# Optimization experiments

Hardware: AMD Instinct MI355X
Metric: run time of the kernel (lower is better)

Reference implementation:

```python
import jax, jax.numpy as jnp
import numpy as np
from jax import lax

D = 256; NH = 8; LYR = 2; G = 64; K = G * G; T = 4; EC = 32
B = 4; N = 512; CITY = 256; DFF = 4 * D

def _conv(x, w):
    return lax.conv_general_dilated(x, w, (1, 1), 'SAME', dimension_numbers=('NCHW', 'OIHW', 'NCHW'))

def _ln(x, w, b):
    m = x.mean(-1, keepdims=True)
    v = ((x - m) ** 2).mean(-1, keepdims=True)
    return (x - m) / jnp.sqrt(v + 1e-5) * w + b

def _mlp(x, w1, b1, w2, b2):
    return jax.nn.gelu(x @ w1 + b1) @ w2 + b2

def setup_inputs():
    key = jax.random.key(0)
    ks = iter(jax.random.split(key, 64))
    def nrm(shape, s=0.02):
        return jax.random.normal(next(ks), shape, jnp.float32) * s
    return {
        'meas_xy': jax.random.uniform(next(ks), (B, N, 2), jnp.float32),
        'meas_v': jax.random.normal(next(ks), (B, N), jnp.float32),
        'bs_xy': jax.random.uniform(next(ks), (B, 1, 2), jnp.float32),
        'task_id': jax.random.randint(next(ks), (B,), 0, T),
        'city': jax.random.uniform(next(ks), (B, CITY, CITY), jnp.float32),
        'mp_w1': nrm((3, D)), 'mp_b1': jnp.zeros((D,)), 'mp_w2': nrm((D, D)), 'mp_b2': jnp.zeros((D,)),
        'bp_w1': nrm((2, D)), 'bp_b1': jnp.zeros((D,)), 'bp_w2': nrm((D, D)), 'bp_b2': jnp.zeros((D,)),
        'env_w1': nrm((EC, 1, 3, 3)), 'env_b1': jnp.zeros((EC,)),
        'env_w2': nrm((EC, EC, 3, 3)), 'env_b2': jnp.zeros((EC,)),
        'env_w3': nrm((D, EC, 1, 1)), 'env_b3': jnp.zeros((D,)),
        'task_emb': nrm((T, D)), 'tp_w': nrm((D, D)), 'tp_b': jnp.zeros((D,)),
        'grid_pos': nrm((K, D)),
        'blk_dens_w': nrm((LYR, D)), 'blk_dens_b': jnp.zeros((LYR, D)),
        'blk_ln1_w': jnp.ones((LYR, D)), 'blk_ln1_b': jnp.zeros((LYR, D)),
        'blk_wq': nrm((LYR, D, D)), 'blk_bq': jnp.zeros((LYR, D)),
        'blk_wk': nrm((LYR, D, D)), 'blk_bk': jnp.zeros((LYR, D)),
        'blk_wv': nrm((LYR, D, D)), 'blk_bv': jnp.zeros((LYR, D)),
        'blk_wo': nrm((LYR, D, D)), 'blk_bo': jnp.zeros((LYR, D)),
        'blk_ln2_w': jnp.ones((LYR, D)), 'blk_ln2_b': jnp.zeros((LYR, D)),
        'blk_ff_w1': nrm((LYR, D, DFF)), 'blk_ff_b1': jnp.zeros((LYR, DFF)),
        'blk_ff_w2': nrm((LYR, DFF, D)), 'blk_ff_b2': jnp.zeros((LYR, D)),
        'tfp_w': nrm((T, D, D)), 'tfp_b': jnp.zeros((T, D)),
        'head_w': nrm((D, 1)), 'head_b': jnp.zeros((1,)),
    }

def reference(meas_xy, meas_v, bs_xy, task_id, city, mp_w1, mp_b1, mp_w2, mp_b2, bp_w1, bp_b1, bp_w2, bp_b2, env_w1, env_b1, env_w2, env_b2, env_w3, env_b3, task_emb, tp_w, tp_b, grid_pos, blk_dens_w, blk_dens_b, blk_ln1_w, blk_ln1_b, blk_wq, blk_bq, blk_wk, blk_bk, blk_wv, blk_bv, blk_wo, blk_bo, blk_ln2_w, blk_ln2_b, blk_ff_w1, blk_ff_b1, blk_ff_w2, blk_ff_b2, tfp_w, tfp_b, head_w, head_b):
    b = meas_xy.shape[0]
    dh = D // NH
    # normalized grid cell centers, [K,2] in (x,y) order
    c = (jnp.arange(G, dtype=jnp.float32) + 0.5) / G
    gy, gx = jnp.meshgrid(c, c, indexing='ij')
    grid_xy = jnp.stack([gx, gy], -1).reshape(K, 2)
    meas_tok = _mlp(jnp.concatenate([meas_xy, meas_v[..., None]], -1), mp_w1, mp_b1, mp_w2, mp_b2)
    bs_tok = _mlp(bs_xy, bp_w1, bp_b1, bp_w2, bp_b2)
    src = jnp.concatenate([meas_tok, bs_tok], 1)       # [B,Ns,D]
    src_xy = jnp.concatenate([meas_xy, bs_xy], 1)      # [B,Ns,2]
    # distance bias: [B,K,Ns]
    attn_bias = -jnp.linalg.norm(grid_xy[None, :, None, :] - src_xy[:, None, :, :], axis=-1)
    # gaussian measurement density: [B,K]
    diff = grid_xy[None, :, None, :] - meas_xy[:, None, :, :]
    dist2 = (diff * diff).sum(-1)
    sigma = 0.08
    density = jnp.exp(-dist2 / (2.0 * sigma * sigma)).mean(-1)
    # env branch: nearest-resize city to GxG, small CNN
    idx = jnp.floor(jnp.arange(G) * (city.shape[1] / G)).astype(jnp.int32)
    city_grid = city[:, idx][:, :, idx][:, None]       # [B,1,G,G]
    h = jax.nn.gelu(_conv(city_grid, env_w1) + env_b1[None, :, None, None])
    h = jax.nn.gelu(_conv(h, env_w2) + env_b2[None, :, None, None])
    env_map = _conv(h, env_w3) + env_b3[None, :, None, None]
    env_grid = env_map.transpose(0, 2, 3, 1).reshape(b, K, D)
    task_vec = (task_emb[task_id] @ tp_w + tp_b)[:, None, :]
    grid = grid_pos[None] + task_vec + env_grid
    inv_sqrt = jnp.float32(1.0 / np.sqrt(dh))
    for l in range(LYR):
        # density modulation injected into the grid latent
        g = grid + density[..., None] * blk_dens_w[l] + blk_dens_b[l]
        hn = _ln(g, blk_ln1_w[l], blk_ln1_b[l])
        q = (hn @ blk_wq[l] + blk_bq[l]).reshape(b, K, NH, dh)
        kk = (src @ blk_wk[l] + blk_bk[l]).reshape(b, -1, NH, dh)
        vv = (src @ blk_wv[l] + blk_bv[l]).reshape(b, -1, NH, dh)
        scores = jnp.einsum('bkhd,bnhd->bhkn', q, kk) * inv_sqrt + attn_bias[:, None]
        a = jax.nn.softmax(scores, -1)
        o = jnp.einsum('bhkn,bnhd->bkhd', a, vv).reshape(b, K, D) @ blk_wo[l] + blk_bo[l]
        g = g + o
        g = g + _mlp(_ln(g, blk_ln2_w[l], blk_ln2_b[l]), blk_ff_w1[l], blk_ff_b1[l], blk_ff_w2[l], blk_ff_b2[l])
        grid = g
    # per-sample task projection from the weight bank
    tf = jax.nn.gelu(jnp.einsum('bkd,bdh->bkh', grid, tfp_w[task_id]) + tfp_b[task_id][:, None, :])
    logits = (tf @ head_w + head_b)[..., 0].reshape(b, G, G)
    return logits
```

## Files before the change

### kernel.cpp

```cpp
#include <hip/hip_runtime.h>
#include <hip/hip_bf16.h>
#include <math.h>

#define D 256
#define NH 8
#define DH 32
#define LYR 2
#define G 64
#define KK 4096
#define T 4
#define EC 32
#define B 4
#define N 512
#define CITY 256
#define DFF 1024
#define NS 513
#define NSP 544
#define MSRC 2052
#define MSRCP 2176
#define ISQ 0.17677669529663687f
#define LOG2E 1.4426950408889634f

typedef short bf16x8 __attribute__((ext_vector_type(8)));
typedef float f32x4 __attribute__((ext_vector_type(4)));

__device__ __forceinline__ float gelu_f(float x) {
    const float c = 0.7978845608028654f;
    float x3 = x * x * x;
    return 0.5f * x * (1.f + tanhf(c * (x + 0.044715f * x3)));
}

__device__ __forceinline__ unsigned short f2bf(float f) {
    unsigned int u = __float_as_uint(f);
    unsigned int r = (u + 0x7FFFu + ((u >> 16) & 1u)) >> 16;
    return (unsigned short)r;
}

__device__ __forceinline__ float bf2f(unsigned short u) {
    return __uint_as_float((unsigned)u << 16);
}

__device__ __forceinline__ unsigned cvtpk(float a, float b) {
    unsigned r;
    asm("v_cvt_pk_bf16_f32 %0, %1, %2" : "=v"(r) : "v"(a), "v"(b));
    return r;
}

__device__ __forceinline__ void gl2lds16(const unsigned short* g, unsigned short* l) {
    __builtin_amdgcn_global_load_lds(
        (const __attribute__((address_space(1))) unsigned int*)g,
        (__attribute__((address_space(3))) unsigned int*)l, 16, 0, 0);
}

__global__ __launch_bounds__(256) void pre1_k(
    const float* __restrict__ wq, const float* __restrict__ wk,
    const float* __restrict__ wv, const float* __restrict__ wo,
    const float* __restrict__ ff1, const float* __restrict__ ff2,
    const float* __restrict__ tfp,
    const float* __restrict__ bk, const float* __restrict__ bv,
    unsigned short* __restrict__ wqT, unsigned short* __restrict__ kvT,
    unsigned short* __restrict__ woT, unsigned short* __restrict__ ff1T,
    unsigned short* __restrict__ ff2T, unsigned short* __restrict__ tfpT,
    float* __restrict__ kvbias,
    const float* __restrict__ meas_xy, const float* __restrict__ meas_v,
    const float* __restrict__ bs_xy,
    const float* __restrict__ mp_w1, const float* __restrict__ mp_b1,
    const float* __restrict__ mp_w2, const float* __restrict__ mp_b2,
    const float* __restrict__ bp_w1, const float* __restrict__ bp_b1,
    const float* __restrict__ bp_w2, const float* __restrict__ bp_b2,
    unsigned short* __restrict__ srcbf, float* __restrict__ src_xy,
    float* __restrict__ dens,
    const float* __restrict__ city, const float* __restrict__ env_w1,
    const float* __restrict__ env_b1, float* __restrict__ h1,
    const float* __restrict__ task_emb, const int* __restrict__ task_id,
    const float* __restrict__ tp_w, const float* __restrict__ tp_b,
    float* __restrict__ tvec,
    unsigned short* __restrict__ khd, unsigned short* __restrict__ vch)
{
    __shared__ float sh[1088];
    int bx = blockIdx.x;
    int tid = threadIdx.x;
    if (bx < 1792) {
        const float* src; unsigned short* dst;
        int Kd, Nn, nmat, rowOff = 0, t; size_t matStride;
        if (bx < 512) {
            int job = bx >> 7; t = bx & 127;
            Kd = 256; Nn = 256; nmat = 2;
            if (job == 0)      { src = wq; dst = wqT; matStride = 65536; }
            else if (job == 1) { src = wk; dst = kvT; matStride = 131072; }
            else if (job == 2) { src = wv; dst = kvT; matStride = 131072; rowOff = 256; }
            else               { src = wo; dst = woT; matStride = 65536; }
            if ((t & 63) == 0 && job == 1) kvbias[(t >> 6) * 512 + tid] = bk[(t >> 6) * 256 + tid];
            if ((t & 63) == 0 && job == 2) kvbias[(t >> 6) * 512 + 256 + tid] = bv[(t >> 6) * 256 + tid];
        } else if (bx < 1024) { t = bx - 512;  src = ff1; dst = ff1T; Kd = 256;  Nn = 1024; nmat = 2; matStride = 262144; }
        else if (bx < 1536)   { t = bx - 1024; src = ff2; dst = ff2T; Kd = 1024; Nn = 256;  nmat = 2; matStride = 262144; }
        else                  { t = bx - 1536; src = tfp; dst = tfpT; Kd = 256;  Nn = 256;  nmat = 4; matStride = 65536; }
        int tn = Nn / 32, perMat = tn * (Kd / 32);
        int mat = t / perMat;
        int rem = t - mat * perMat;
        int nb = (rem % tn) * 32, kb = (rem / tn) * 32;
        const float* s = src + (size_t)mat * Kd * Nn;
        unsigned short* d = dst + (size_t)mat * matStride;
        float (*tb)[33] = (float (*)[33])sh;
        int tx = tid & 31, ty = tid >> 5;
        #pragma unroll
        for (int i = 0; i < 4; i++)
            tb[ty + i * 8][tx] = s[(size_t)(kb + ty + i * 8) * Nn + nb + tx];
        __syncthreads();
        #pragma unroll
        for (int i = 0; i < 4; i++)
            d[(size_t)(rowOff + nb + ty + i * 8) * Kd + kb + tx] = f2bf(tb[tx][ty + i * 8]);
    } else if (bx < 3968) {
        int id = bx - 1792;
        int dd = tid;
        if (id >= B * N + B) {
            srcbf[(size_t)id * D + dd] = 0;
            return;
        }
        float* hid = sh;
        int row;
        const float *w1, *b1, *w2, *b2;
        float x0, x1, x2 = 0.f;
        int nin;
        if (id < B * N) {
            int b = id >> 9, n = id & 511;
            x0 = meas_xy[(b * N + n) * 2 + 0];
            x1 = meas_xy[(b * N + n) * 2 + 1];
            x2 = meas_v[b * N + n];
            w1 = mp_w1; b1 = mp_b1; w2 = mp_w2; b2 = mp_b2; nin = 3;
            row = b * NS + n;
        } else {
            int b = id - B * N;
            x0 = bs_xy[b * 2 + 0];
            x1 = bs_xy[b * 2 + 1];
            w1 = bp_w1; b1 = bp_b1; w2 = bp_w2; b2 = bp_b2; nin = 2;
            row = b * NS + N;
        }
        float h = x0 * w1[dd] + x1 * w1[D + dd] + b1[dd];
        if (nin == 3) h += x2 * w1[2 * D + dd];
        hid[dd] = gelu_f(h);
        __syncthreads();
        float o = b2[dd];
        for (int j = 0; j < D; j++) o += hid[j] * w2[j * D + dd];
        srcbf[(size_t)row * D + dd] = f2bf(o);
        if (dd == 0) { src_xy[row * 2 + 0] = x0; src_xy[row * 2 + 1] = x1; }
    } else if (bx < 4032) {
        int blk = bx - 3968;
        int b = blk >> 4, kc = blk & 15;
        int k = kc * 256 + tid;
        float* mx = sh; float* my = sh + 512;
        for (int i = tid; i < N; i += 256) {
            mx[i] = meas_xy[(b * N + i) * 2 + 0];
            my[i] = meas_xy[(b * N + i) * 2 + 1];
        }
        __syncthreads();
        float gx = ((k & 63) + 0.5f) / 64.f;
        float gy = ((k >> 6) + 0.5f) / 64.f;
        float s = 0.f;
        for (int n = 0; n < N; n++) {
            float dx = gx - mx[n], dy = gy - my[n];
            s += __expf(-(dx * dx + dy * dy) * 78.125f);
        }
        dens[b * KK + k] = s * (1.f / (float)N);
    } else if (bx < 6080) {
        int i = (bx - 4032) * 256 + tid;
        int x = i & 63, y = (i >> 6) & 63, c = (i >> 12) & 31, b = i >> 17;
        float s = env_b1[c];
        for (int ky = 0; ky < 3; ky++) {
            int yy = y + ky - 1;
            if (yy < 0 || yy >= G) continue;
            for (int kx = 0; kx < 3; kx++) {
                int xx = x + kx - 1;
                if (xx < 0 || xx >= G) continue;
                s += city[(b * CITY + yy * 4) * CITY + xx * 4] * env_w1[c * 9 + ky * 3 + kx];
            }
        }
        h1[i] = gelu_f(s);
    } else if (bx < 6084) {
        int b = bx - 6080;
        float* e = sh;
        e[tid] = task_emb[task_id[b] * D + tid];
        __syncthreads();
        float s = tp_b[tid];
        for (int j = 0; j < D; j++) s += e[j] * tp_w[j * D + tid];
        tvec[b * D + tid] = s;
    } else {
        int bh = bx - 6084;
        unsigned short* kp = khd + ((size_t)bh * 544 + 513) * 32;
        for (int i = tid; i < 992; i += 256) kp[i] = 0;
        unsigned short* vp = vch + ((size_t)bh * 17 + 16) * 1024;
        for (int i = tid; i < 1024; i += 256) vp[i] = 0;
    }
}

__global__ __launch_bounds__(256) void conv2_k(
    const float* __restrict__ h1, const float* __restrict__ w,
    const float* __restrict__ bias, float* __restrict__ h2) {
    int blk = blockIdx.x;
    int yt = blk & 15, cg = (blk >> 4) & 7, b = blk >> 7;
    int x = threadIdx.x & 63, y = yt * 4 + (threadIdx.x >> 6);
    int c0 = cg * 4;
    float flag[9];
    int off[9];
    #pragma unroll
    for (int ky = 0; ky < 3; ky++) {
        int yy = y + ky - 1;
        bool vy = (yy >= 0 && yy < G);
        int yc = min(max(yy, 0), G - 1);
        #pragma unroll
        for (int kx = 0; kx < 3; kx++) {
            int xx = x + kx - 1;
            bool vx = (xx >= 0 && xx < G);
            int xc = min(max(xx, 0), G - 1);
            flag[ky * 3 + kx] = (vy && vx) ? 1.f : 0.f;
            off[ky * 3 + kx] = yc * G + xc;
        }
    }
    const float* hp = h1 + ((size_t)(b * EC) << 12);
    float acc[4] = {bias[c0], bias[c0 + 1], bias[c0 + 2], bias[c0 + 3]};
    float v[9], nv[9];
    #pragma unroll
    for (int t = 0; t < 9; t++) v[t] = hp[off[t]] * flag[t];
    for (int ci = 0; ci < EC; ci++) {
        if (ci < EC - 1) {
            const float* hn = hp + ((size_t)(ci + 1) << 12);
            #pragma unroll
            for (int t = 0; t < 9; t++) nv[t] = hn[off[t]] * flag[t];
        }
        #pragma unroll
        for (int cc = 0; cc < 4; cc++) {
            const float* wp = w + ((size_t)(c0 + cc) * EC + ci) * 9;
            #pragma unroll
            for (int t = 0; t < 9; t++) acc[cc] += v[t] * wp[t];
        }
        #pragma unroll
        for (int t = 0; t < 9; t++) v[t] = nv[t];
    }
    size_t obase = (((size_t)(b * EC + c0)) << 12) + y * G + x;
    #pragma unroll
    for (int cc = 0; cc < 4; cc++)
        h2[obase + ((size_t)cc << 12)] = gelu_f(acc[cc]);
}

__global__ __launch_bounds__(256) void pre2_k(
    const float* __restrict__ h2, const float* __restrict__ w3,
    const float* __restrict__ b3, const float* __restrict__ grid_pos,
    const float* __restrict__ tvec, float* __restrict__ grid,
    const float* __restrict__ sxy, unsigned short* __restrict__ nd,
    float* __restrict__ out, const float* __restrict__ head_b)
{
    __shared__ float sh[1088];
    int bx = blockIdx.x;
    int tid = threadIdx.x;
    if (bx < 2048) {
        int b = bx >> 9, k0 = (bx & 511) * 8;
        float (*h2s)[8] = (float (*)[8])sh;
        h2s[tid >> 3][tid & 7] = h2[(((size_t)b * EC + (tid >> 3)) << 12) + k0 + (tid & 7)];
        float w3r[32];
        #pragma unroll
        for (int c4 = 0; c4 < 8; c4++) {
            float4 w4 = *(const float4*)(w3 + tid * 32 + c4 * 4);
            w3r[c4 * 4 + 0] = w4.x; w3r[c4 * 4 + 1] = w4.y;
            w3r[c4 * 4 + 2] = w4.z; w3r[c4 * 4 + 3] = w4.w;
        }
        float base = b3[tid] + tvec[b * D + tid];
        __syncthreads();
        #pragma unroll
        for (int j = 0; j < 8; j++) {
            float s = base + grid_pos[(size_t)(k0 + j) * D + tid];
            #pragma unroll
            for (int ci = 0; ci < 32; ci++) s += h2s[ci][j] * w3r[ci];
            grid[((size_t)b * KK + k0 + j) * D + tid] = s;
        }
    } else if (bx < 2304) {
        int q = bx - 2048;
        int b = q >> 6, qt = q & 63;
        float* sxs = sh; float* sys = sh + 544;
        for (int i = tid; i < 544; i += 256) {
            float x = 0.f, y = 0.f;
            if (i < NS) { x = sxy[(b * NS + i) * 2]; y = sxy[(b * NS + i) * 2 + 1]; }
            sxs[i] = x; sys[i] = y;
        }
        __syncthreads();
        unsigned short* base = nd + (size_t)q * 34816;
        for (int c = 0; c < 17; c++) {
            #pragma unroll
            for (int it = 0; it < 2; it++) {
                int lin = it * 256 + tid;
                int w16 = lin & 63, q4 = (lin >> 6) & 3, half = lin >> 8;
                int qidx = qt * 64 + w16;
                float gx = ((qidx & 63) + 0.5f) * (1.f / 64.f);
                float gy = ((qidx >> 6) + 0.5f) * (1.f / 64.f);
                unsigned short vs[4];
                #pragma unroll
                for (int r = 0; r < 4; r++) {
                    int tok = c * 32 + half * 16 + q4 * 4 + r;
                    float val;
                    if (tok < NS) {
                        float dx = gx - sxs[tok], dy = gy - sys[tok];
                        val = -sqrtf(dx * dx + dy * dy);
                    } else val = -1e4f;
                    vs[r] = f2bf(val * LOG2E);
                }
                ushort4 o; o.x = vs[0]; o.y = vs[1]; o.z = vs[2]; o.w = vs[3];
                *(ushort4*)(base + (size_t)c * 2048 + lin * 4) = o;
            }
        }
    } else {
        out[(bx - 2304) * 256 + tid] = head_b[0];
    }
}

template <int DENS>
__global__ __launch_bounds__(256) void dens_ln_k(
    float* __restrict__ grid, const float* __restrict__ dens,
    const float* __restrict__ dw, const float* __restrict__ db,
    const float* __restrict__ lw, const float* __restrict__ lb,
    unsigned short* __restrict__ y) {
    int row = blockIdx.x * 4 + (threadIdx.x >> 6);
    int lane = threadIdx.x & 63;
    float* gp = grid + (size_t)row * D + lane * 4;
    float4 v = *(float4*)gp;
    if (DENS) {
        float de = dens[row];
        float4 w4 = *(const float4*)(dw + lane * 4);
        float4 b4 = *(const float4*)(db + lane * 4);
        v.x += de * w4.x + b4.x; v.y += de * w4.y + b4.y;
        v.z += de * w4.z + b4.z; v.w += de * w4.w + b4.w;
        *(float4*)gp = v;
    }
    float s = v.x + v.y + v.z + v.w;
    #pragma unroll
    for (int o = 32; o > 0; o >>= 1) s += __shfl_xor(s, o);
    float mean = s * (1.f / D);
    float cx = v.x - mean, cy = v.y - mean, cz = v.z - mean, cw = v.w - mean;
    float q = cx * cx + cy * cy + cz * cz + cw * cw;
    #pragma unroll
    for (int o = 32; o > 0; o >>= 1) q += __shfl_xor(q, o);
    float inv = rsqrtf(q * (1.f / D) + 1e-5f);
    float4 lwv = *(const float4*)(lw + lane * 4);
    float4 lbv = *(const float4*)(lb + lane * 4);
    ushort4 o4;
    o4.x = f2bf(cx * inv * lwv.x + lbv.x);
    o4.y = f2bf(cy * inv * lwv.y + lbv.y);
    o4.z = f2bf(cz * inv * lwv.z + lbv.z);
    o4.w = f2bf(cw * inv * lwv.w + lbv.w);
    *(ushort4*)(y + (size_t)row * D + lane * 4) = o4;
}

template <int GELU, int ACCUM, int OBF, int TFPH, int STBF, int KVT = 0>
__device__ __forceinline__ void gemm_core(
    const unsigned short* __restrict__ A, const unsigned short* __restrict__ Wt,
    const float* __restrict__ bias, void* __restrict__ Cv,
    int M, int K, int Nn, int bn, int bm,
    const float* __restrict__ hw, unsigned short* __restrict__ Xb, float scale,
    unsigned short* As, unsigned short* Bs) {
    int tid = threadIdx.x;
    int wave = tid >> 6, lane = tid & 63;
    int q4 = lane >> 4, lr = lane & 15;
    int wn = wave * 16;
    int srow = tid >> 2, sk8 = (tid & 3) * 8;
    const unsigned short* Ap  = A  + (size_t)(bm + srow) * K + sk8;
    const unsigned short* Bp0 = Wt + (size_t)(bn + srow) * K + sk8;
    unsigned short* AsD = As + tid * 8;
    unsigned short* BsD = Bs + tid * 8;
    f32x4 acc[4] = {};

    gl2lds16(Ap,       AsD);
    gl2lds16(Ap + 32,  AsD + 2048);
    gl2lds16(Bp0,      BsD);
    gl2lds16(Bp0 + 32, BsD + 2048);

    int nk = K >> 6;
    for (int ki = 0; ki < nk; ki++) {
        __syncthreads();
        if (ki + 1 < nk) {
            int k0 = (ki + 1) << 6;
            int nb = ((ki + 1) & 1) * 4096;
            gl2lds16(Ap + k0,       AsD + nb);
            gl2lds16(Ap + k0 + 32,  AsD + nb + 2048);
            gl2lds16(Bp0 + k0,      BsD + nb);
            gl2lds16(Bp0 + k0 + 32, BsD + nb + 2048);
        }
        int cb = (ki & 1) * 4096;
        #pragma unroll
        for (int ks = 0; ks < 2; ks++) {
            bf16x8 af[4], bf;
            #pragma unroll
            for (int i = 0; i < 4; i++)
                af[i] = *(const bf16x8*)&As[cb + ks * 2048 + (i * 16 + lr) * 32 + q4 * 8];
            bf = *(const bf16x8*)&Bs[cb + ks * 2048 + (wn + lr) * 32 + q4 * 8];
            #pragma unroll
            for (int i = 0; i < 4; i++)
                acc[i] = __builtin_amdgcn_mfma_f32_16x16x32_bf16(af[i], bf, acc[i], 0, 0, 0);
        }
    }

    if (KVT) {
        int gc = bn + wn + lr;
        float bv = bias[gc];
        bool isV = gc >= 256;
        #pragma unroll
        for (int i = 0; i < 4; i++) {
            #pragma unroll
            for (int r = 0; r < 4; r++) {
                int gr = bm + i * 16 + q4 * 4 + r;
                if (gr < MSRC) {
                    float v = acc[i][r] + bv;
                    int bb = gr / NS;
                    int tok = gr - bb * NS;
                    if (!isV) {
                        int h = gc >> 5, dh = gc & 31;
                        ((unsigned short*)Cv)[(((size_t)(bb * 8 + h) * 544) + tok) * 32 + dh] = f2bf(v);
                    } else {
                        int gcv = gc - 256;
                        int h = gcv >> 5, dh = gcv & 31;
                        int c = tok >> 5, t32 = tok & 31;
                        Xb[((((size_t)(bb * 8 + h) * 17 + c) * 32 + dh)) * 32 + t32] = f2bf(v);
                    }
                }
            }
        }
        return;
    }

    if (TFPH) {
        int gc = bn + wn + lr;
        float bv = bias[gc];
        float hv = hw[gc];
        #pragma unroll
        for (int i = 0; i < 4; i++) {
            #pragma unroll
            for (int r = 0; r < 4; r++) {
                float s = gelu_f(acc[i][r] + bv) * hv;
                s += __shfl_xor(s, 1); s += __shfl_xor(s, 2);
                s += __shfl_xor(s, 4); s += __shfl_xor(s, 8);
                if (lr == 0)
                    atomicAdd((float*)Cv + (bm + i * 16 + q4 * 4 + r), s);
            }
        }
        return;
    }

    int gc = bn + wn + lr;
    float bv = bias[gc];
    #pragma unroll
    for (int i = 0; i < 4; i++) {
        #pragma unroll
        for (int r = 0; r < 4; r++) {
            int gr = bm + i * 16 + q4 * 4 + r;
            if (gr < M) {
                float v = (acc[i][r] + bv) * scale;
                if (GELU) v = gelu_f(v);
                size_t idx = (size_t)gr * Nn + gc;
                if (OBF) {
                    ((unsigned short*)Cv)[idx] = f2bf(v);
                } else if (ACCUM) {
                    float nv = ((float*)Cv)[idx] + v;
                    ((float*)Cv)[idx] = nv;
                    if (STBF) Xb[idx] = f2bf(nv);
                } else {
                    ((float*)Cv)[idx] = v;
                }
            }
        }
    }
}

template <int GELU, int ACCUM, int OBF, int TFPH, int STBF>
__global__ __launch_bounds__(256) void gemm_k(
    const unsigned short* __restrict__ A, const unsigned short* __restrict__ Wt0,
    const float* __restrict__ bias0, void* __restrict__ Cv,
    int M, int K, int Nn, const int* __restrict__ task_id,
    const float* __restrict__ hw, unsigned short* __restrict__ Xb) {
    __shared__ unsigned short As[8192];
    __shared__ unsigned short Bs[8192];
    const unsigned short* Wt = Wt0;
    const float* bias = bias0;
    int bm = blockIdx.y * 64;
    if (TFPH) { int t = task_id[bm >> 12]; Wt += (size_t)t * D * D; bias += t * D; }
    gemm_core<GELU, ACCUM, OBF, TFPH, STBF>(A, Wt, bias, Cv, M, K, Nn,
                                            blockIdx.x * 64, bm, hw, Xb, 1.f, As, Bs);
}

__global__ __launch_bounds__(256) void qkv_k(
    const unsigned short* __restrict__ xbf, const unsigned short* __restrict__ wqT,
    const float* __restrict__ bq, unsigned short* __restrict__ qbf,
    const unsigned short* __restrict__ srcbf, const unsigned short* __restrict__ kvT,
    const float* __restrict__ kvb, unsigned short* __restrict__ khd,
    unsigned short* __restrict__ vch) {
    __shared__ unsigned short As[8192];
    __shared__ unsigned short Bs[8192];
    if (blockIdx.x < 4) {
        gemm_core<0, 0, 1, 0, 0, 0>(xbf, wqT, bq, qbf, B * KK, D, D,
                                    blockIdx.x * 64, blockIdx.y * 64, nullptr, nullptr,
                                    ISQ * LOG2E, As, Bs);
    } else {
        if (blockIdx.y >= MSRCP / 64) return;
        gemm_core<0, 0, 1, 0, 0, 1>(srcbf, kvT, kvb, khd, MSRC, D, 512,
                                    (blockIdx.x - 4) * 64, blockIdx.y * 64, nullptr, vch, 1.f, As, Bs);
    }
}

__global__ __launch_bounds__(256) void attn_mfma(
    const unsigned short* __restrict__ qb,
    const unsigned short* __restrict__ khd,
    const unsigned short* __restrict__ vch,
    const unsigned short* __restrict__ ndL,
    unsigned short* __restrict__ out)
{
    int bid = blockIdx.x;
    int qt = bid & 63, h = (bid >> 6) & 7, b = bid >> 9;
    int tid = threadIdx.x, wave = tid >> 6, lane = tid & 63;
    int q4 = lane >> 4, lr = lane & 15;

    int kbase = qt * 64 + wave * 16;
    size_t qrow = (size_t)(b * KK + kbase + lr);
    bf16x8 qf = *(const bf16x8*)(qb + qrow * D + h * DH + q4 * 8);
    const unsigned short* kp0 = khd + ((size_t)(b * 8 + h) * 544) * 32 + lr * 32 + q4 * 8;
    const unsigned short* vb0 = vch + ((size_t)(b * 8 + h) * 17) * 1024 + lr * 32 + q4 * 8;
    const unsigned short* ndp = ndL + ((size_t)(b * 64 + qt)) * 34816 + q4 * 256 + (wave * 16 + lr) * 4;

    float ll0 = 0.f, ll1 = 0.f;
    f32x4 o0 = {0.f, 0.f, 0.f, 0.f}, o1 = {0.f, 0.f, 0.f, 0.f};
    int sA = ((lane >> 4) & 1) * 32 + lr;
    int sB = sA + 16;
    bool hi = (lane & 32) != 0;

    bf16x8 kf0 = *(const bf16x8*)kp0;
    bf16x8 kf1 = *(const bf16x8*)(kp0 + 512);
    bf16x8 vt0 = *(const bf16x8*)vb0;
    bf16x8 vt1 = *(const bf16x8*)(vb0 + 512);
    ushort4 n0v = *(const ushort4*)ndp;
    ushort4 n1v = *(const ushort4*)(ndp + 1024);

    for (int c = 0; c < 17; c++) {
        bf16x8 ck0 = kf0, ck1 = kf1, cv0 = vt0, cv1 = vt1;
        ushort4 cn0 = n0v, cn1 = n1v;
        if (c < 16) {
            size_t co = (size_t)(c + 1) * 1024;
            kf0 = *(const bf16x8*)(kp0 + co);
            kf1 = *(const bf16x8*)(kp0 + co + 512);
            vt0 = *(const bf16x8*)(vb0 + co);
            vt1 = *(const bf16x8*)(vb0 + co + 512);
            n0v = *(const ushort4*)(ndp + (size_t)(c + 1) * 2048);
            n1v = *(const ushort4*)(ndp + (size_t)(c + 1) * 2048 + 1024);
        }
        f32x4 s0 = {0.f, 0.f, 0.f, 0.f}, s1 = {0.f, 0.f, 0.f, 0.f};
        s0 = __builtin_amdgcn_mfma_f32_16x16x32_bf16(ck0, qf, s0, 0, 0, 0);
        s1 = __builtin_amdgcn_mfma_f32_16x16x32_bf16(ck1, qf, s1, 0, 0, 0);
        float p0[4], p1[4];
        p0[0] = __builtin_amdgcn_exp2f(s0[0] + bf2f(cn0.x));
        p0[1] = __builtin_amdgcn_exp2f(s0[1] + bf2f(cn0.y));
        p0[2] = __builtin_amdgcn_exp2f(s0[2] + bf2f(cn0.z));
        p0[3] = __builtin_amdgcn_exp2f(s0[3] + bf2f(cn0.w));
        p1[0] = __builtin_amdgcn_exp2f(s1[0] + bf2f(cn1.x));
        p1[1] = __builtin_amdgcn_exp2f(s1[1] + bf2f(cn1.y));
        p1[2] = __builtin_amdgcn_exp2f(s1[2] + bf2f(cn1.z));
        p1[3] = __builtin_amdgcn_exp2f(s1[3] + bf2f(cn1.w));
        ll0 += (p0[0] + p0[1]) + (p0[2] + p0[3]);
        ll1 += (p1[0] + p1[1]) + (p1[2] + p1[3]);
        unsigned pk0 = cvtpk(p0[0], p0[1]);
        unsigned pk1 = cvtpk(p0[2], p0[3]);
        unsigned pk2 = cvtpk(p1[0], p1[1]);
        unsigned pk3 = cvtpk(p1[2], p1[3]);
        unsigned a0 = (unsigned)__shfl((int)pk0, sA), c0 = (unsigned)__shfl((int)pk2, sA);
        unsigned a1 = (unsigned)__shfl((int)pk1, sA), c1 = (unsigned)__shfl((int)pk3, sA);
        unsigned a2 = (unsigned)__shfl((int)pk0, sB), c2 = (unsigned)__shfl((int)pk2, sB);
        unsigned a3 = (unsigned)__shfl((int)pk1, sB), c3 = (unsigned)__shfl((int)pk3, sB);
        union { unsigned u[4]; bf16x8 v; } pu;
        pu.u[0] = hi ? c0 : a0;
        pu.u[1] = hi ? c1 : a1;
        pu.u[2] = hi ? c2 : a2;
        pu.u[3] = hi ? c3 : a3;
        o0 = __builtin_amdgcn_mfma_f32_16x16x32_bf16(cv0, pu.v, o0, 0, 0, 0);
        o1 = __builtin_amdgcn_mfma_f32_16x16x32_bf16(cv1, pu.v, o1, 0, 0, 0);
    }

    float ll = ll0 + ll1;
    ll += __shfl_xor(ll, 16);
    ll += __shfl_xor(ll, 32);
    float inv = 1.f / ll;
    unsigned w0 = cvtpk(o0[0] * inv, o0[1] * inv);
    unsigned w1 = cvtpk(o0[2] * inv, o0[3] * inv);
    unsigned w2 = cvtpk(o1[0] * inv, o1[1] * inv);
    unsigned w3 = cvtpk(o1[2] * inv, o1[3] * inv);
    uint2 st0; st0.x = w0; st0.y = w1;
    uint2 st1; st1.x = w2; st1.y = w3;
    *(uint2*)(out + qrow * D + h * DH + q4 * 4) = st0;
    *(uint2*)(out + qrow * D + h * DH + 16 + q4 * 4) = st1;
}

extern "C" void kernel_launch(void* const* d_in, const int* in_sizes, int n_in,
                              void* d_out, int out_size, void* d_ws, size_t ws_size,
                              hipStream_t stream) {
    const float* meas_xy = (const float*)d_in[0];
    const float* meas_v  = (const float*)d_in[1];
    const float* bs_xy   = (const float*)d_in[2];
    const int*   task_id = (const int*)d_in[3];
    const float* city    = (const float*)d_in[4];
    const float* mp_w1 = (const float*)d_in[5];  const float* mp_b1 = (const float*)d_in[6];
    const float* mp_w2 = (const float*)d_in[7];  const float* mp_b2 = (const float*)d_in[8];
    const float* bp_w1 = (const float*)d_in[9];  const float* bp_b1 = (const float*)d_in[10];
    const float* bp_w2 = (const float*)d_in[11]; const float* bp_b2 = (const float*)d_in[12];
    const float* env_w1 = (const float*)d_in[13]; const float* env_b1 = (const float*)d_in[14];
    const float* env_w2 = (const float*)d_in[15]; const float* env_b2 = (const float*)d_in[16];
    const float* env_w3 = (const float*)d_in[17]; const float* env_b3 = (const float*)d_in[18];
    const float* task_emb = (const float*)d_in[19];
    const float* tp_w = (const float*)d_in[20]; const float* tp_b = (const float*)d_in[21];
    const float* grid_pos = (const float*)d_in[22];
    const float* dens_w = (const float*)d_in[23]; const float* dens_b = (const float*)d_in[24];
    const float* ln1_w = (const float*)d_in[25]; const float* ln1_b = (const float*)d_in[26];
    const float* wq = (const float*)d_in[27]; const float* bq = (const float*)d_in[28];
    const float* wk = (const float*)d_in[29]; const float* bk = (const float*)d_in[30];
    const float* wv = (const float*)d_in[31]; const float* bv = (const float*)d_in[32];
    const float* wo = (const float*)d_in[33]; const float* bo = (const float*)d_in[34];
    const float* ln2_w = (const float*)d_in[35]; const float* ln2_b = (const float*)d_in[36];
    const float* ff_w1 = (const float*)d_in[37]; const float* ff_b1 = (const float*)d_in[38];
    const float* ff_w2 = (const float*)d_in[39]; const float* ff_b2 = (const float*)d_in[40];
    const float* tfp_w = (const float*)d_in[41]; const float* tfp_b = (const float*)d_in[42];
    const float* head_w = (const float*)d_in[43]; const float* head_b = (const float*)d_in[44];
    float* out = (float*)d_out;

    float* ws = (float*)d_ws;
    size_t off = 0;
    float* src_xy = ws + off; off += (size_t)B * NS * 2 + 128;
    float* dens   = ws + off; off += (size_t)B * KK;
    float* tvec   = ws + off; off += (size_t)B * D;
    float* h1     = ws + off; off += (size_t)B * EC * KK;
    float* grid   = ws + off; off += (size_t)B * KK * D;
    unsigned short* srcbf = (unsigned short*)(ws + off); off += (size_t)MSRCP * D / 2;
    unsigned short* khd   = (unsigned short*)(ws + off); off += (size_t)B * 8 * 544 * 32 / 2;
    unsigned short* vch   = (unsigned short*)(ws + off); off += (size_t)B * 8 * 17 * 1024 / 2;
    float* qreg   = ws + off; off += (size_t)B * KK * D / 2;
    unsigned short* qbf = (unsigned short*)qreg;
    float* h2     = qreg;
    unsigned short* xbf    = (unsigned short*)(ws + off); off += (size_t)B * KK * D / 2;
    unsigned short* attnbf = (unsigned short*)(ws + off); off += (size_t)B * KK * D / 2;
    unsigned short* ndbf   = (unsigned short*)(ws + off); off += (size_t)B * 64 * 34816 / 2;
    unsigned short* hidbf  = (unsigned short*)(ws + off); off += (size_t)B * KK * DFF / 2;
    unsigned short* wqT  = (unsigned short*)(ws + off); off += (size_t)LYR * D * D / 2;
    unsigned short* kvT  = (unsigned short*)(ws + off); off += (size_t)LYR * 512 * D / 2;
    unsigned short* woT  = (unsigned short*)(ws + off); off += (size_t)LYR * D * D / 2;
    unsigned short* ff1T = (unsigned short*)(ws + off); off += (size_t)LYR * D * DFF / 2;
    unsigned short* ff2T = (unsigned short*)(ws + off); off += (size_t)LYR * DFF * D / 2;
    unsigned short* tfpT = (unsigned short*)(ws + off); off += (size_t)T * D * D / 2;
    float* kvbias = ws + off; off += (size_t)LYR * 512;
    (void)ws_size; (void)n_in; (void)in_sizes; (void)out_size;

    const int M = B * KK;

    pre1_k<<<6116, 256, 0, stream>>>(
        wq, wk, wv, wo, ff_w1, ff_w2, tfp_w, bk, bv,
        wqT, kvT, woT, ff1T, ff2T, tfpT, kvbias,
        meas_xy, meas_v, bs_xy, mp_w1, mp_b1, mp_w2, mp_b2,
        bp_w1, bp_b1, bp_w2, bp_b2, srcbf, src_xy,
        dens, city, env_w1, env_b1, h1,
        task_emb, task_id, tp_w, tp_b, tvec, khd, vch);
    conv2_k<<<512, 256, 0, stream>>>(h1, env_w2, env_b2, h2);
    pre2_k<<<2368, 256, 0, stream>>>(h2, env_w3, env_b3, grid_pos, tvec, grid,
                                     src_xy, ndbf, out, head_b);

    for (int l = 0; l < LYR; l++) {
        dens_ln_k<1><<<M / 4, 256, 0, stream>>>(grid, dens, dens_w + l * D, dens_b + l * D,
                                                ln1_w + l * D, ln1_b + l * D, xbf);
        qkv_k<<<dim3(12, 256), 256, 0, stream>>>(
            xbf, wqT + (size_t)l * D * D, bq + l * D, qbf,
            srcbf, kvT + (size_t)l * 512 * D, kvbias + l * 512, khd, vch);
        attn_mfma<<<B * NH * 64, 256, 0, stream>>>(qbf, khd, vch, ndbf, attnbf);
        gemm_k<0, 1, 0, 0, 0><<<dim3(4, 256), 256, 0, stream>>>(
            attnbf, woT + (size_t)l * D * D, bo + l * D, grid, M, D, D, nullptr, nullptr, nullptr);
        dens_ln_k<0><<<M / 4, 256, 0, stream>>>(grid, nullptr, nullptr, nullptr,
                                                ln2_w + l * D, ln2_b + l * D, xbf);
        gemm_k<1, 0, 1, 0, 0><<<dim3(16, 256), 256, 0, stream>>>(
            xbf, ff1T + (size_t)l * D * DFF, ff_b1 + l * DFF, hidbf, M, D, DFF,
            nullptr, nullptr, nullptr);
        if (l == 0) {
            gemm_k<0, 1, 0, 0, 0><<<dim3(4, 256), 256, 0, stream>>>(
                hidbf, ff2T + (size_t)l * DFF * D, ff_b2 + l * D, grid, M, DFF, D,
                nullptr, nullptr, nullptr);
        } else {
            gemm_k<0, 1, 0, 0, 1><<<dim3(4, 256), 256, 0, stream>>>(
                hidbf, ff2T + (size_t)l * DFF * D, ff_b2 + l * D, grid, M, DFF, D,
                nullptr, nullptr, xbf);
        }
    }
    gemm_k<1, 0, 0, 1, 0><<<dim3(4, 256), 256, 0, stream>>>(
        xbf, tfpT, tfp_b, out, M, D, D, task_id, head_w, nullptr);
}
```

Before: 578.2 us.

## Permute K token layout to drop P shuffles and double-buffer attention loads

Keys and the density-bias table are now stored in a permuted token order. This lets the softmax probabilities from the score MFMA feed straight into the PV MFMA B operand, so the eight cross-lane shuffles and selects per chunk go away. The attention loop is also unrolled by two with ping-pong register buffers, giving a prefetch distance of two chunks. The cost is higher register pressure, and the K-write and bias-table producers must match the new permutation exactly.

```diff
diff --git a/kernel.cpp b/kernel.cpp
--- a/kernel.cpp
+++ b/kernel.cpp
@@ -294,7 +294,7 @@
                 unsigned short vs[4];
                 #pragma unroll
                 for (int r = 0; r < 4; r++) {
-                    int tok = c * 32 + half * 16 + q4 * 4 + r;
+                    int tok = c * 32 + q4 * 8 + 2 * r + half;
                     float val;
                     if (tok < NS) {
                         float dx = gx - sxs[tok], dy = gy - sys[tok];
@@ -411,7 +411,10 @@
                     int tok = gr - bb * NS;
                     if (!isV) {
                         int h = gc >> 5, dh = gc & 31;
-                        ((unsigned short*)Cv)[(((size_t)(bb * 8 + h) * 544) + tok) * 32 + dh] = f2bf(v);
+                        int t32 = tok & 31;
+                        int kkp = ((t32 & 1) << 4) | ((t32 >> 3) << 2) | ((t32 >> 1) & 3);
+                        int tokP = (tok & ~31) | kkp;
+                        ((unsigned short*)Cv)[(((size_t)(bb * 8 + h) * 544) + tokP) * 32 + dh] = f2bf(v);
                     } else {
                         int gcv = gc - 256;
                         int h = gcv >> 5, dh = gcv & 31;
@@ -523,59 +526,59 @@
 
     float ll0 = 0.f, ll1 = 0.f;
     f32x4 o0 = {0.f, 0.f, 0.f, 0.f}, o1 = {0.f, 0.f, 0.f, 0.f};
-    int sA = ((lane >> 4) & 1) * 32 + lr;
-    int sB = sA + 16;
-    bool hi = (lane & 32) != 0;
-
-    bf16x8 kf0 = *(const bf16x8*)kp0;
-    bf16x8 kf1 = *(const bf16x8*)(kp0 + 512);
-    bf16x8 vt0 = *(const bf16x8*)vb0;
-    bf16x8 vt1 = *(const bf16x8*)(vb0 + 512);
-    ushort4 n0v = *(const ushort4*)ndp;
-    ushort4 n1v = *(const ushort4*)(ndp + 1024);
-
-    for (int c = 0; c < 17; c++) {
-        bf16x8 ck0 = kf0, ck1 = kf1, cv0 = vt0, cv1 = vt1;
-        ushort4 cn0 = n0v, cn1 = n1v;
-        if (c < 16) {
-            size_t co = (size_t)(c + 1) * 1024;
-            kf0 = *(const bf16x8*)(kp0 + co);
-            kf1 = *(const bf16x8*)(kp0 + co + 512);
-            vt0 = *(const bf16x8*)(vb0 + co);
-            vt1 = *(const bf16x8*)(vb0 + co + 512);
-            n0v = *(const ushort4*)(ndp + (size_t)(c + 1) * 2048);
-            n1v = *(const ushort4*)(ndp + (size_t)(c + 1) * 2048 + 1024);
-        }
-        f32x4 s0 = {0.f, 0.f, 0.f, 0.f}, s1 = {0.f, 0.f, 0.f, 0.f};
-        s0 = __builtin_amdgcn_mfma_f32_16x16x32_bf16(ck0, qf, s0, 0, 0, 0);
-        s1 = __builtin_amdgcn_mfma_f32_16x16x32_bf16(ck1, qf, s1, 0, 0, 0);
-        float p0[4], p1[4];
-        p0[0] = __builtin_amdgcn_exp2f(s0[0] + bf2f(cn0.x));
-        p0[1] = __builtin_amdgcn_exp2f(s0[1] + bf2f(cn0.y));
-        p0[2] = __builtin_amdgcn_exp2f(s0[2] + bf2f(cn0.z));
-        p0[3] = __builtin_amdgcn_exp2f(s0[3] + bf2f(cn0.w));
-        p1[0] = __builtin_amdgcn_exp2f(s1[0] + bf2f(cn1.x));
-        p1[1] = __builtin_amdgcn_exp2f(s1[1] + bf2f(cn1.y));
-        p1[2] = __builtin_amdgcn_exp2f(s1[2] + bf2f(cn1.z));
-        p1[3] = __builtin_amdgcn_exp2f(s1[3] + bf2f(cn1.w));
-        ll0 += (p0[0] + p0[1]) + (p0[2] + p0[3]);
-        ll1 += (p1[0] + p1[1]) + (p1[2] + p1[3]);
-        unsigned pk0 = cvtpk(p0[0], p0[1]);
-        unsigned pk1 = cvtpk(p0[2], p0[3]);
-        unsigned pk2 = cvtpk(p1[0], p1[1]);
-        unsigned pk3 = cvtpk(p1[2], p1[3]);
-        unsigned a0 = (unsigned)__shfl((int)pk0, sA), c0 = (unsigned)__shfl((int)pk2, sA);
-        unsigned a1 = (unsigned)__shfl((int)pk1, sA), c1 = (unsigned)__shfl((int)pk3, sA);
-        unsigned a2 = (unsigned)__shfl((int)pk0, sB), c2 = (unsigned)__shfl((int)pk2, sB);
-        unsigned a3 = (unsigned)__shfl((int)pk1, sB), c3 = (unsigned)__shfl((int)pk3, sB);
-        union { unsigned u[4]; bf16x8 v; } pu;
-        pu.u[0] = hi ? c0 : a0;
-        pu.u[1] = hi ? c1 : a1;
-        pu.u[2] = hi ? c2 : a2;
-        pu.u[3] = hi ? c3 : a3;
-        o0 = __builtin_amdgcn_mfma_f32_16x16x32_bf16(cv0, pu.v, o0, 0, 0, 0);
-        o1 = __builtin_amdgcn_mfma_f32_16x16x32_bf16(cv1, pu.v, o1, 0, 0, 0);
-    }
+
+    bf16x8 k0X, k1X, v0X, v1X, k0Y, k1Y, v0Y, v1Y;
+    ushort4 n0X, n1X, n0Y, n1Y;
+
+#define LDK(S, c) { size_t co = (size_t)(c) * 1024; \
+    k0##S = *(const bf16x8*)(kp0 + co); k1##S = *(const bf16x8*)(kp0 + co + 512); }
+#define LDV(S, c) { size_t co = (size_t)(c) * 1024; \
+    v0##S = *(const bf16x8*)(vb0 + co); v1##S = *(const bf16x8*)(vb0 + co + 512); }
+#define LDN(S, c) { size_t no = (size_t)(c) * 2048; \
+    n0##S = *(const ushort4*)(ndp + no); n1##S = *(const ushort4*)(ndp + no + 1024); }
+
+    LDK(X, 0); LDV(X, 0); LDN(X, 0);
+    LDK(Y, 1); LDV(Y, 1); LDN(Y, 1);
+
+#define BODY(S, cp) { \
+    f32x4 s0 = {0.f, 0.f, 0.f, 0.f}, s1 = {0.f, 0.f, 0.f, 0.f}; \
+    s0 = __builtin_amdgcn_mfma_f32_16x16x32_bf16(k0##S, qf, s0, 0, 0, 0); \
+    s1 = __builtin_amdgcn_mfma_f32_16x16x32_bf16(k1##S, qf, s1, 0, 0, 0); \
+    LDK(S, cp); \
+    float p0[4], p1[4]; \
+    p0[0] = __builtin_amdgcn_exp2f(s0[0] + bf2f(n0##S.x)); \
+    p0[1] = __builtin_amdgcn_exp2f(s0[1] + bf2f(n0##S.y)); \
+    p0[2] = __builtin_amdgcn_exp2f(s0[2] + bf2f(n0##S.z)); \
+    p0[3] = __builtin_amdgcn_exp2f(s0[3] + bf2f(n0##S.w)); \
+    p1[0] = __builtin_amdgcn_exp2f(s1[0] + bf2f(n1##S.x)); \
+    p1[1] = __builtin_amdgcn_exp2f(s1[1] + bf2f(n1##S.y)); \
+    p1[2] = __builtin_amdgcn_exp2f(s1[2] + bf2f(n1##S.z)); \
+    p1[3] = __builtin_amdgcn_exp2f(s1[3] + bf2f(n1##S.w)); \
+    LDN(S, cp); \
+    ll0 += (p0[0] + p0[1]) + (p0[2] + p0[3]); \
+    ll1 += (p1[0] + p1[1]) + (p1[2] + p1[3]); \
+    union { unsigned u[4]; bf16x8 v; } pu; \
+    pu.u[0] = cvtpk(p0[0], p1[0]); \
+    pu.u[1] = cvtpk(p0[1], p1[1]); \
+    pu.u[2] = cvtpk(p0[2], p1[2]); \
+    pu.u[3] = cvtpk(p0[3], p1[3]); \
+    o0 = __builtin_amdgcn_mfma_f32_16x16x32_bf16(v0##S, pu.v, o0, 0, 0, 0); \
+    o1 = __builtin_amdgcn_mfma_f32_16x16x32_bf16(v1##S, pu.v, o1, 0, 0, 0); \
+    LDV(S, cp); \
+}
+
+    for (int c = 0; c < 16; c += 2) {
+        int cpX = c + 2;
+        int cpY = (c + 3 > 16) ? 16 : c + 3;
+        BODY(X, cpX);
+        BODY(Y, cpY);
+    }
+    BODY(X, 16);
+
+#undef BODY
+#undef LDK
+#undef LDV
+#undef LDN
 
     float ll = ll0 + ll1;
     ll += __shfl_xor(ll, 16);
```

Result: slower. 608.4 us (+5.2%).
